# Optimization experiments

Measured on AMD Instinct MI355X. Metric: run time of the kernel, lower is better.

## Reference

```python
import jax, jax.numpy as jnp
import numpy as np

N = 100000
IN_DIM = 128
OUT_DIM = 128
E = 320000


def setup_inputs() -> dict:
    key = jax.random.key(0)
    ks = jax.random.split(key, 12)
    x = jax.random.normal(ks[0], (N, IN_DIM), dtype=jnp.float32)
    src0 = jax.random.randint(ks[1], (E,), 0, N)
    dst0 = jax.random.randint(ks[2], (E,), 0, N)
    src1 = jax.random.randint(ks[3], (E,), 0, N)
    dst1 = jax.random.randint(ks[4], (E,), 0, N)
    s = 1.0 / np.sqrt(IN_DIM)
    W0 = jax.random.uniform(ks[5], (IN_DIM, OUT_DIM), minval=-s, maxval=s)
    b0 = jax.random.uniform(ks[6], (OUT_DIM,), minval=-s, maxval=s)
    W1 = jax.random.uniform(ks[7], (IN_DIM, OUT_DIM), minval=-s, maxval=s)
    b1 = jax.random.uniform(ks[8], (OUT_DIM,), minval=-s, maxval=s)
    sa = 1.0 / np.sqrt(2 * OUT_DIM)
    a0 = jax.random.uniform(ks[9], (2 * OUT_DIM,), minval=-sa, maxval=sa)
    a1 = jax.random.uniform(ks[10], (2 * OUT_DIM,), minval=-sa, maxval=sa)
    return {"x": x, "src0": src0, "dst0": dst0, "src1": src1, "dst1": dst1,
            "W0": W0, "b0": b0, "a0": a0, "W1": W1, "b1": b1, "a1": a1}


def _rel_gat(x, src, dst, W, b, a):
    # wh = Linear(in_dim, out_dim)(x)  -> [N, D]
    wh = x @ W + b
    D = wh.shape[1]
    # e = leaky_relu(a^T [wh_src || wh_dst]) ; split a instead of concat on edges
    e = jax.nn.leaky_relu(wh[src] @ a[:D] + wh[dst] @ a[D:])  # [E]
    # segment softmax over incoming edges of each dst node
    m = jax.ops.segment_max(e, dst, num_segments=N)
    ex = jnp.exp(e - m[dst])
    denom = jax.ops.segment_sum(ex, dst, num_segments=N)
    alpha = ex / denom[dst]  # [E]
    # weighted scatter-sum of src features (zero for isolated dst nodes)
    return jax.ops.segment_sum(alpha[:, None] * wh[src], dst, num_segments=N)


def reference(x, src0, dst0, src1, dst1, W0, b0, a0, W1, b1, a1):
    h0 = _rel_gat(x, src0, dst0, W0, b0, a0)
    h1 = _rel_gat(x, src1, dst1, W1, b1, a1)
    # cross-relation 'sum' reducer
    return h0 + h1
```

## Files before the change

kernel.cpp:

```cpp
#include <hip/hip_runtime.h>
#include <hip/hip_bf16.h>


typedef __bf16 bf16x8 __attribute__((ext_vector_type(8)));
typedef float f32x4 __attribute__((ext_vector_type(4)));

#define DIM 128

__global__ __launch_bounds__(256) void prep_w_kernel(
    const float* __restrict__ W0, const float* __restrict__ W1,
    __bf16* __restrict__ wtf)
{
    const int e = blockIdx.x * 256 + threadIdx.x;
    if (e >= 4096) return;
    const int lane = e & 63;
    const int ko4  = (e >> 6) & 3;
    const int ct   = (e >> 8) & 7;
    const int rel  = e >> 11;
    const float* W = rel ? W1 : W0;
    const int n  = ct * 16 + (lane & 15);
    const int k0 = ko4 * 32 + (lane >> 4) * 8;
    bf16x8 v;
#pragma unroll
    for (int j = 0; j < 8; ++j) v[j] = (__bf16)W[(k0 + j) * DIM + n];
    *(bf16x8*)(wtf + (size_t)e * 8) = v;
}

__global__ __launch_bounds__(256) void gemm_wh_kernel(
    const float* __restrict__ x, const __bf16* __restrict__ wtf,
    const float* __restrict__ b0, const float* __restrict__ b1,
    const float* __restrict__ a0, const float* __restrict__ a1,
    const int* __restrict__ dst0, const int* __restrict__ dst1,
    unsigned* __restrict__ deg,
    __bf16* __restrict__ wh, float* __restrict__ s_src,
    float* __restrict__ s_dst, int N, int E)
{
    __shared__ __align__(16) __bf16 Cst[64 * 136];
    const int tid = threadIdx.x;

    {
        const int gid = blockIdx.x * 256 + tid;
        if (gid < E) {
            atomicAdd(deg + dst0[gid], 1u);
            atomicAdd(deg + N + dst1[gid], 1u);
        }
    }

    const int lane = tid & 63;
    const int wave = tid >> 6;
    const int quad = lane >> 4;
    const int mr   = lane & 15;

    const long row0 = (long)blockIdx.x * 64 + wave * 16;
    long arow = row0 + mr;
    if (arow >= N) arow = N - 1;
    const f32x4* xr = (const f32x4*)(x + arow * DIM);

    bf16x8 afrag[4];
#pragma unroll
    for (int ko4 = 0; ko4 < 4; ++ko4) {
        f32x4 lo = xr[ko4 * 8 + quad * 2], hi = xr[ko4 * 8 + quad * 2 + 1];
        afrag[ko4] = (bf16x8){ (__bf16)lo.x, (__bf16)lo.y, (__bf16)lo.z, (__bf16)lo.w,
                               (__bf16)hi.x, (__bf16)hi.y, (__bf16)hi.z, (__bf16)hi.w };
    }

    const bf16x8* wt = (const bf16x8*)wtf;

#pragma unroll
    for (int rel = 0; rel < 2; ++rel) {
        f32x4 zero = {0.f, 0.f, 0.f, 0.f};
        f32x4 acc[8];
#pragma unroll
        for (int t = 0; t < 8; ++t) acc[t] = zero;

#pragma unroll
        for (int ko4 = 0; ko4 < 4; ++ko4) {
#pragma unroll
            for (int ct = 0; ct < 8; ++ct) {
                bf16x8 bfrag = wt[((rel * 8 + ct) * 4 + ko4) * 64 + lane];
                acc[ct] = __builtin_amdgcn_mfma_f32_16x16x32_bf16(afrag[ko4], bfrag, acc[ct], 0, 0, 0);
            }
        }

        const float* bias = rel ? b1 : b0;
        const float* a    = rel ? a1 : a0;
        float psr[4] = {0.f, 0.f, 0.f, 0.f};
        float pdr[4] = {0.f, 0.f, 0.f, 0.f};
#pragma unroll
        for (int ct = 0; ct < 8; ++ct) {
            const int c = ct * 16 + mr;
            const float bn = bias[c];
            const float asc = a[c], adc = a[DIM + c];
#pragma unroll
            for (int rr = 0; rr < 4; ++rr) {
                const float wv = acc[ct][rr] + bn;
                Cst[(wave * 16 + quad * 4 + rr) * 136 + c] = (__bf16)wv;
                psr[rr] += asc * wv;
                pdr[rr] += adc * wv;
            }
        }
#pragma unroll
        for (int off = 1; off < 16; off <<= 1) {
#pragma unroll
            for (int rr = 0; rr < 4; ++rr) {
                psr[rr] += __shfl_xor(psr[rr], off);
                pdr[rr] += __shfl_xor(pdr[rr], off);
            }
        }
        if (mr == 0) {
#pragma unroll
            for (int rr = 0; rr < 4; ++rr) {
                const long orow = row0 + quad * 4 + rr;
                if (orow < N) {
                    s_src[(size_t)rel * N + orow] = psr[rr];
                    s_dst[(size_t)rel * N + orow] = pdr[rr];
                }
            }
        }
        __syncthreads();
#pragma unroll
        for (int i = 0; i < 4; ++i) {
            const int chunk = tid + 256 * i;
            const int row = chunk >> 4, c8 = chunk & 15;
            bf16x8 v = *(const bf16x8*)&Cst[row * 136 + c8 * 8];
            const long grow = (long)blockIdx.x * 64 + row;
            if (grow < N)
                *(bf16x8*)(wh + ((size_t)rel * N + grow) * DIM + c8 * 8) = v;
        }
        __syncthreads();
    }
}

__global__ __launch_bounds__(256) void scanA_kernel(
    const unsigned* __restrict__ deg, unsigned* __restrict__ tmp,
    unsigned* __restrict__ bsum, int n)
{
    __shared__ unsigned s[256];
    const int t = threadIdx.x;
    const int i = blockIdx.x * 256 + t;
    unsigned v = (i < n) ? deg[i] : 0u;
    s[t] = v;
    __syncthreads();
#pragma unroll
    for (int off = 1; off < 256; off <<= 1) {
        unsigned add = (t >= off) ? s[t - off] : 0u;
        __syncthreads();
        s[t] += add;
        __syncthreads();
    }
    if (i < n) tmp[i] = s[t] - v;
    if (t == 255) bsum[blockIdx.x] = s[t];
}

__global__ __launch_bounds__(256) void scan2_kernel(
    const unsigned* __restrict__ tmp, const unsigned* __restrict__ bsum,
    const unsigned* __restrict__ deg, unsigned* __restrict__ rowptr,
    unsigned* __restrict__ cursor, int n, int nb)
{
    __shared__ unsigned s[256];
    __shared__ unsigned ex[1024];
    const int t = threadIdx.x;
    unsigned loc[4], sum = 0u;
#pragma unroll
    for (int k = 0; k < 4; ++k) {
        int idx = t * 4 + k;
        loc[k] = (idx < nb) ? bsum[idx] : 0u;
        sum += loc[k];
    }
    s[t] = sum;
    __syncthreads();
#pragma unroll
    for (int off = 1; off < 256; off <<= 1) {
        unsigned add = (t >= off) ? s[t - off] : 0u;
        __syncthreads();
        s[t] += add;
        __syncthreads();
    }
    unsigned run = s[t] - sum;
#pragma unroll
    for (int k = 0; k < 4; ++k) {
        ex[t * 4 + k] = run;
        run += loc[k];
    }
    __syncthreads();
    const unsigned pref = ex[blockIdx.x];
    const int i = blockIdx.x * 256 + t;
    if (i < n) {
        unsigned val = tmp[i] + pref;
        rowptr[i] = val;
        cursor[i] = val;
        if (i == n - 1) rowptr[n] = val + deg[i];
    }
}

__global__ __launch_bounds__(256) void fill_kernel(
    const int* __restrict__ src0, const int* __restrict__ dst0,
    const int* __restrict__ src1, const int* __restrict__ dst1,
    unsigned* __restrict__ cursor, unsigned* __restrict__ sorted_src,
    int N, int E)
{
    int i = blockIdx.x * 256 + threadIdx.x;
    if (i >= E) return;
    unsigned p0 = atomicAdd(cursor + dst0[i], 1u);
    sorted_src[p0] = (unsigned)src0[i];
    unsigned p1 = atomicAdd(cursor + N + dst1[i], 1u);
    sorted_src[p1] = (unsigned)src1[i];
}

__global__ __launch_bounds__(256) void aggregate_kernel(
    const unsigned* __restrict__ rowptr, const unsigned* __restrict__ sorted_src,
    const float* __restrict__ s_src, const float* __restrict__ s_dst,
    const __bf16* __restrict__ wh, float* __restrict__ out, int N)
{
    const int tid  = threadIdx.x;
    const int lane = tid & 63;
    const int sub  = lane >> 4;
    const int mr   = lane & 15;
    const int d    = blockIdx.x * 4 + (tid >> 6);
    if (d >= N) return;

    float o[8];
#pragma unroll
    for (int k = 0; k < 8; ++k) o[k] = 0.f;

#pragma unroll
    for (int r = 0; r < 2; ++r) {
        const int base = r * N + d;
        const unsigned beg = rowptr[base], end = rowptr[base + 1];
        if (beg == end) continue;
        const float sd = s_dst[base];
        const float* ss = s_src + (size_t)r * N;
        const __bf16* whr = wh + (size_t)r * N * DIM;

        float l = 0.f, a[8];
#pragma unroll
        for (int k = 0; k < 8; ++k) a[k] = 0.f;

        for (unsigned j0 = beg; j0 < end; j0 += 4) {
            const unsigned j = j0 + sub;
            const bool ok = j < end;
            const unsigned s = ok ? sorted_src[j] : 0u;
            float v = ss[s] + sd;
            v = v > 0.f ? v : 0.01f * v;
            const float e = ok ? __expf(v) : 0.f;
            bf16x8 w = *(const bf16x8*)(whr + (size_t)s * DIM + mr * 8);
            l += e;
#pragma unroll
            for (int k = 0; k < 8; ++k) a[k] += e * (float)w[k];
        }
        l += __shfl_xor(l, 16); l += __shfl_xor(l, 32);
#pragma unroll
        for (int k = 0; k < 8; ++k) {
            a[k] += __shfl_xor(a[k], 16);
            a[k] += __shfl_xor(a[k], 32);
        }
        const float inv = 1.f / l;
#pragma unroll
        for (int k = 0; k < 8; ++k) o[k] += a[k] * inv;
    }

    if (sub == 0) {
        float4 v0 = {o[0], o[1], o[2], o[3]};
        float4 v1 = {o[4], o[5], o[6], o[7]};
        float* op = out + (size_t)d * DIM + mr * 8;
        *(float4*)op       = v0;
        *(float4*)(op + 4) = v1;
    }
}

extern "C" void kernel_launch(void* const* d_in, const int* in_sizes, int n_in,
                              void* d_out, int out_size, void* d_ws, size_t ws_size,
                              hipStream_t stream) {
    const float* x = (const float*)d_in[0];
    const int* srcs[2] = {(const int*)d_in[1], (const int*)d_in[3]};
    const int* dsts[2] = {(const int*)d_in[2], (const int*)d_in[4]};
    const float* Ws[2] = {(const float*)d_in[5], (const float*)d_in[8]};
    const float* Bs[2] = {(const float*)d_in[6], (const float*)d_in[9]};
    const float* As[2] = {(const float*)d_in[7], (const float*)d_in[10]};

    const int N = in_sizes[0] / DIM;
    const int E = in_sizes[1];
    const int n2 = 2 * N;
    const int nb = (n2 + 255) / 256;
    float* out = (float*)d_out;

    char* p = (char*)d_ws;
    __bf16*   wh     = (__bf16*)p;   p += (size_t)n2 * DIM * 2;
    __bf16*   wtf    = (__bf16*)p;   p += (size_t)4096 * 8 * 2;
    float*    s_src  = (float*)p;    p += (size_t)n2 * 4;
    float*    s_dst  = (float*)p;    p += (size_t)n2 * 4;
    unsigned* deg    = (unsigned*)p; p += (size_t)n2 * 4;
    unsigned* tmp    = (unsigned*)p; p += (size_t)n2 * 4;
    unsigned* rowptr = (unsigned*)p; p += (size_t)(n2 + 1) * 4;
    unsigned* cursor = (unsigned*)p; p += (size_t)n2 * 4;
    unsigned* ssrc   = (unsigned*)p; p += (size_t)2 * E * 4;
    unsigned* bsum   = (unsigned*)p; p += (size_t)nb * 4;

    hipMemsetAsync(deg, 0, (size_t)n2 * 4, stream);
    prep_w_kernel<<<16, 256, 0, stream>>>(Ws[0], Ws[1], wtf);

    gemm_wh_kernel<<<(N + 63) / 64, 256, 0, stream>>>(
        x, wtf, Bs[0], Bs[1], As[0], As[1],
        dsts[0], dsts[1], deg, wh, s_src, s_dst, N, E);

    scanA_kernel<<<nb, 256, 0, stream>>>(deg, tmp, bsum, n2);
    scan2_kernel<<<nb, 256, 0, stream>>>(tmp, bsum, deg, rowptr, cursor, n2, nb);
    fill_kernel<<<(E + 255) / 256, 256, 0, stream>>>(
        srcs[0], dsts[0], srcs[1], dsts[1], cursor, ssrc, N, E);
    aggregate_kernel<<<(N + 3) / 4, 256, 0, stream>>>(
        rowptr, ssrc, s_src, s_dst, wh, out, N);
}
```

Before: 262.5 us.

## Precompute edge softmax weights in fill and merge relations in aggregate loop

The fill kernel now computes each edge's leaky-relu exponent, atomically accumulates the softmax denominator per destination, and stores (src, weight) pairs in the CSR array. The aggregate kernel no longer gathers s_src per edge. It treats both relations' edges as a single stream, processes 8 edges per iteration for more memory-level parallelism, and needs only one final cross-lane reduction. In exchange it adds float atomics on the denominators, doubles the size of the sorted array, and makes the summation order nondeterministic. It also skips the max subtraction in the softmax, which could overflow for large logits.

```diff
diff --git a/kernel.cpp b/kernel.cpp
--- a/kernel.cpp
+++ b/kernel.cpp
@@ -196,67 +196,87 @@
 __global__ __launch_bounds__(256) void fill_kernel(
     const int* __restrict__ src0, const int* __restrict__ dst0,
     const int* __restrict__ src1, const int* __restrict__ dst1,
-    unsigned* __restrict__ cursor, unsigned* __restrict__ sorted_src,
-    int N, int E)
-{
-    int i = blockIdx.x * 256 + threadIdx.x;
+    const float* __restrict__ s_src, const float* __restrict__ s_dst,
+    unsigned* __restrict__ cursor, float* __restrict__ denom,
+    uint2* __restrict__ sorted, int N, int E)
+{
+    const int i = blockIdx.x * 256 + threadIdx.x;
     if (i >= E) return;
-    unsigned p0 = atomicAdd(cursor + dst0[i], 1u);
-    sorted_src[p0] = (unsigned)src0[i];
-    unsigned p1 = atomicAdd(cursor + N + dst1[i], 1u);
-    sorted_src[p1] = (unsigned)src1[i];
+    const int s0 = src0[i], d0 = dst0[i];
+    const int s1 = src1[i], d1 = dst1[i];
+
+    float v0 = s_src[s0] + s_dst[d0];
+    v0 = v0 > 0.f ? v0 : 0.01f * v0;
+    const float e0 = __expf(v0);
+    float v1 = s_src[N + s1] + s_dst[N + d1];
+    v1 = v1 > 0.f ? v1 : 0.01f * v1;
+    const float e1 = __expf(v1);
+
+    atomicAdd(denom + d0, e0);
+    const unsigned p0 = atomicAdd(cursor + d0, 1u);
+    sorted[p0] = make_uint2((unsigned)s0, __float_as_uint(e0));
+
+    atomicAdd(denom + N + d1, e1);
+    const unsigned p1 = atomicAdd(cursor + N + d1, 1u);
+    sorted[p1] = make_uint2((unsigned)s1, __float_as_uint(e1));
 }
 
 __global__ __launch_bounds__(256) void aggregate_kernel(
-    const unsigned* __restrict__ rowptr, const unsigned* __restrict__ sorted_src,
-    const float* __restrict__ s_src, const float* __restrict__ s_dst,
-    const __bf16* __restrict__ wh, float* __restrict__ out, int N)
+    const unsigned* __restrict__ rowptr, const uint2* __restrict__ sorted,
+    const float* __restrict__ denom, const __bf16* __restrict__ wh,
+    float* __restrict__ out, int N)
 {
     const int tid  = threadIdx.x;
     const int lane = tid & 63;
     const int sub  = lane >> 4;
     const int mr   = lane & 15;
-    const int d    = blockIdx.x * 4 + (tid >> 6);
+    int d = blockIdx.x * 4 + (tid >> 6);
     if (d >= N) return;
+    d = __builtin_amdgcn_readfirstlane(d);
+
+    const unsigned beg0 = rowptr[d],     end0 = rowptr[d + 1];
+    const unsigned beg1 = rowptr[N + d], end1 = rowptr[N + d + 1];
+    const unsigned len0 = end0 - beg0;
+    const unsigned T    = len0 + (end1 - beg1);
+    const float inv0 = (end0 > beg0) ? 1.f / denom[d]     : 0.f;
+    const float inv1 = (end1 > beg1) ? 1.f / denom[N + d] : 0.f;
 
     float o[8];
 #pragma unroll
     for (int k = 0; k < 8; ++k) o[k] = 0.f;
 
-#pragma unroll
-    for (int r = 0; r < 2; ++r) {
-        const int base = r * N + d;
-        const unsigned beg = rowptr[base], end = rowptr[base + 1];
-        if (beg == end) continue;
-        const float sd = s_dst[base];
-        const float* ss = s_src + (size_t)r * N;
-        const __bf16* whr = wh + (size_t)r * N * DIM;
-
-        float l = 0.f, a[8];
-#pragma unroll
-        for (int k = 0; k < 8; ++k) a[k] = 0.f;
-
-        for (unsigned j0 = beg; j0 < end; j0 += 4) {
-            const unsigned j = j0 + sub;
-            const bool ok = j < end;
-            const unsigned s = ok ? sorted_src[j] : 0u;
-            float v = ss[s] + sd;
-            v = v > 0.f ? v : 0.01f * v;
-            const float e = ok ? __expf(v) : 0.f;
-            bf16x8 w = *(const bf16x8*)(whr + (size_t)s * DIM + mr * 8);
-            l += e;
-#pragma unroll
-            for (int k = 0; k < 8; ++k) a[k] += e * (float)w[k];
-        }
-        l += __shfl_xor(l, 16); l += __shfl_xor(l, 32);
-#pragma unroll
-        for (int k = 0; k < 8; ++k) {
-            a[k] += __shfl_xor(a[k], 16);
-            a[k] += __shfl_xor(a[k], 32);
-        }
-        const float inv = 1.f / l;
-#pragma unroll
-        for (int k = 0; k < 8; ++k) o[k] += a[k] * inv;
+    const size_t whstride = (size_t)N * DIM;
+
+    for (unsigned t0 = 0; t0 < T; t0 += 8) {
+        const unsigned tA = t0 + sub, tB = tA + 4;
+        const bool vA = tA < T, vB = tB < T;
+        const bool rA = tA >= len0, rB = tB >= len0;
+
+        unsigned iA = rA ? beg1 + (tA - len0) : beg0 + tA;
+        unsigned iB = rB ? beg1 + (tB - len0) : beg0 + tB;
+        iA = vA ? iA : 0u;
+        iB = vB ? iB : 0u;
+
+        const uint2 eA = sorted[iA];
+        const uint2 eB = sorted[iB];
+
+        const float wgtA = vA ? __uint_as_float(eA.y) * (rA ? inv1 : inv0) : 0.f;
+        const float wgtB = vB ? __uint_as_float(eB.y) * (rB ? inv1 : inv0) : 0.f;
+
+        const bf16x8 wA = *(const bf16x8*)(wh + (rA ? whstride : 0)
+                                              + (size_t)eA.x * DIM + mr * 8);
+        const bf16x8 wB = *(const bf16x8*)(wh + (rB ? whstride : 0)
+                                              + (size_t)eB.x * DIM + mr * 8);
+#pragma unroll
+        for (int k = 0; k < 8; ++k) o[k] += wgtA * (float)wA[k];
+#pragma unroll
+        for (int k = 0; k < 8; ++k) o[k] += wgtB * (float)wB[k];
+    }
+
+#pragma unroll
+    for (int k = 0; k < 8; ++k) {
+        o[k] += __shfl_xor(o[k], 16);
+        o[k] += __shfl_xor(o[k], 32);
     }
 
     if (sub == 0) {
@@ -290,13 +310,14 @@
     float*    s_src  = (float*)p;    p += (size_t)n2 * 4;
     float*    s_dst  = (float*)p;    p += (size_t)n2 * 4;
     unsigned* deg    = (unsigned*)p; p += (size_t)n2 * 4;
+    float*    denom  = (float*)p;    p += (size_t)n2 * 4;
     unsigned* tmp    = (unsigned*)p; p += (size_t)n2 * 4;
-    unsigned* rowptr = (unsigned*)p; p += (size_t)(n2 + 1) * 4;
+    unsigned* rowptr = (unsigned*)p; p += (size_t)(n2 + 2) * 4;
     unsigned* cursor = (unsigned*)p; p += (size_t)n2 * 4;
-    unsigned* ssrc   = (unsigned*)p; p += (size_t)2 * E * 4;
+    uint2*    sorted = (uint2*)p;    p += (size_t)2 * E * 8;
     unsigned* bsum   = (unsigned*)p; p += (size_t)nb * 4;
 
-    hipMemsetAsync(deg, 0, (size_t)n2 * 4, stream);
+    hipMemsetAsync(deg, 0, (size_t)n2 * 4 * 2, stream);
     prep_w_kernel<<<16, 256, 0, stream>>>(Ws[0], Ws[1], wtf);
 
     gemm_wh_kernel<<<(N + 63) / 64, 256, 0, stream>>>(
@@ -306,7 +327,8 @@
     scanA_kernel<<<nb, 256, 0, stream>>>(deg, tmp, bsum, n2);
     scan2_kernel<<<nb, 256, 0, stream>>>(tmp, bsum, deg, rowptr, cursor, n2, nb);
     fill_kernel<<<(E + 255) / 256, 256, 0, stream>>>(
-        srcs[0], dsts[0], srcs[1], dsts[1], cursor, ssrc, N, E);
+        srcs[0], dsts[0], srcs[1], dsts[1], s_src, s_dst,
+        cursor, denom, sorted, N, E);
     aggregate_kernel<<<(N + 3) / 4, 256, 0, stream>>>(
-        rowptr, ssrc, s_src, s_dst, wh, out, N);
-}
+        rowptr, sorted, denom, wh, out, N);
+}
```

Result: no change. 267.4 us (+1.9%).
